# Kernel tuning notes

Hardware: AMD Instinct MI355X
Metric: run time of the kernel (lower is better)

The kernel has to match this reference:

```python
import jax, jax.numpy as jnp
import numpy as np

B, T, C = 2, 2048, 2048
H, KV, D = 16, 4, 128   # n_head, n_kv_head, head_dim
EPS = 1.1920929e-07     # torch.finfo(float32).eps, F.rms_norm default


def setup_inputs() -> dict:
    key = jax.random.key(0)
    ks = jax.random.split(key, 7)
    x = jax.random.normal(ks[0], (B, T, C), dtype=jnp.float32)
    # rope angles: cos/sin of positions, broadcastable to [B,T,H,D//2]
    inv_freq = 1.0 / (10000.0 ** (jnp.arange(0, D // 2, dtype=jnp.float32) / (D // 2)))
    ang = jnp.arange(T, dtype=jnp.float32)[:, None] * inv_freq[None, :]
    cos = jnp.cos(ang)[None, :, None, :]  # [1,T,1,D/2]
    sin = jnp.sin(ang)[None, :, None, :]
    s = 0.02
    Wq = jax.random.normal(ks[1], (C, H * D), dtype=jnp.float32) * s
    Wk = jax.random.normal(ks[2], (C, KV * D), dtype=jnp.float32) * s
    Wv = jax.random.normal(ks[3], (C, KV * D), dtype=jnp.float32) * s
    Wo = jax.random.normal(ks[4], (C, C), dtype=jnp.float32) * s
    return {"x": x, "cos": cos, "sin": sin, "Wq": Wq, "Wk": Wk, "Wv": Wv, "Wo": Wo}


def _rope(t, cos, sin):
    d = t.shape[-1] // 2
    t1, t2 = t[..., :d], t[..., d:]
    return jnp.concatenate([t1 * cos + t2 * sin, -t1 * sin + t2 * cos], axis=-1)


def _rmsnorm(t):
    return t * jax.lax.rsqrt(jnp.mean(t * t, axis=-1, keepdims=True) + EPS)


def reference(x, cos, sin, Wq, Wk, Wv, Wo):
    q = (x @ Wq).reshape(B, T, H, D)
    k = (x @ Wk).reshape(B, T, KV, D)
    v = (x @ Wv).reshape(B, T, KV, D)
    q = _rmsnorm(_rope(q, cos, sin))
    k = _rmsnorm(_rope(k, cos, sin))
    # [B, KV, G, T, D] query grouped per kv head (GQA)
    G = H // KV
    qh = q.transpose(0, 2, 1, 3).reshape(B, KV, G, T, D)
    kh = k.transpose(0, 2, 1, 3)  # [B, KV, T, D]
    vh = v.transpose(0, 2, 1, 3)
    scale = 1.0 / np.sqrt(D).astype(np.float32)
    scores = jnp.einsum('bhgqd,bhkd->bhgqk', qh, kh) * scale
    causal = jnp.tril(jnp.ones((T, T), dtype=bool))
    scores = jnp.where(causal, scores, jnp.finfo(scores.dtype).min)
    attn = jax.nn.softmax(scores, axis=-1)
    y = jnp.einsum('bhgqk,bhkd->bhgqd', attn, vh)  # [B,KV,G,T,D]
    y = y.reshape(B, H, T, D).transpose(0, 2, 1, 3).reshape(B, T, C)
    return y @ Wo
```

## Files before the change

### kernel.cpp

```cpp
#include <hip/hip_runtime.h>

using bf16x8 = __attribute__((ext_vector_type(8))) short;
using f32x4  = __attribute__((ext_vector_type(4))) float;

#define B_  2
#define T_  2048
#define C_  2048
#define H_  16
#define KV_ 4
#define D_  128

__device__ __forceinline__ unsigned short f2b(float f) {
  union { float f; unsigned int u; } v; v.f = f;
  unsigned int r = v.u + 0x7fffu + ((v.u >> 16) & 1u);
  return (unsigned short)(r >> 16);
}
__device__ __forceinline__ float b2f(unsigned short u) {
  union { unsigned int u; float f; } v; v.u = ((unsigned int)u) << 16;
  return v.f;
}
__device__ __forceinline__ unsigned int cvt_pk_bf16(float lo, float hi) {
  unsigned int r;
  asm("v_cvt_pk_bf16_f32 %0, %1, %2" : "=v"(r) : "v"(lo), "v"(hi));
  return r;
}
__device__ __forceinline__ void gld_lds16(const void* g, void* l) {
  __builtin_amdgcn_global_load_lds(
      (__attribute__((address_space(1))) void*)g,
      (__attribute__((address_space(3))) void*)l, 16, 0, 0);
}

__global__ void cast_bf16_k(const float* __restrict__ in, unsigned short* __restrict__ out) {
  int i = blockIdx.x * 256 + threadIdx.x;
  float4 f = ((const float4*)in)[i];
  ushort4 u; u.x = f2b(f.x); u.y = f2b(f.y); u.z = f2b(f.z); u.w = f2b(f.w);
  ((ushort4*)out)[i] = u;
}

__global__ void wtrans(const float* __restrict__ W, unsigned short* __restrict__ Wt,
                       int K, int N) {
  __shared__ float s[32][33];
  int n0 = blockIdx.x * 32, k0 = blockIdx.y * 32;
  int tx = threadIdx.x, ty = threadIdx.y;
  #pragma unroll
  for (int yy = 0; yy < 32; yy += 8)
    s[ty + yy][tx] = W[(size_t)(k0 + ty + yy) * N + n0 + tx];
  __syncthreads();
  #pragma unroll
  for (int yy = 0; yy < 32; yy += 8)
    Wt[(size_t)(n0 + ty + yy) * K + k0 + tx] = f2b(s[tx][ty + yy]);
}

template <bool OUT_BF16>
__device__ __forceinline__ void gemm_tile(
    const unsigned short* __restrict__ A, const unsigned short* __restrict__ Bt,
    void* __restrict__ Cv, int K, int ldc, int m0, int n0b, int n0c,
    unsigned short* sA, unsigned short* sB)
{
  const int tid  = threadIdx.x;
  const int lane = tid & 63, w = tid >> 6;
  const int quad = lane >> 4, l16 = lane & 15;
  const int wm = (w >> 1) * 64, wn = (w & 1) * 64;

  f32x4 acc[4][4] = {};

  const unsigned short* Abase = A  + (size_t)m0  * K;
  const unsigned short* Bbase = Bt + (size_t)n0b * K;

  for (int k0 = 0; k0 < K; k0 += 32) {
    #pragma unroll
    for (int r = 0; r < 2; ++r) {
      int c = tid + r * 256;
      int row = c >> 2, col = (c & 3) * 8;
      gld_lds16(Abase + (size_t)row * K + k0 + col, sA + c * 8);
      gld_lds16(Bbase + (size_t)row * K + k0 + col, sB + c * 8);
    }
    __syncthreads();
    bf16x8 af[4], bfr[4];
    #pragma unroll
    for (int i = 0; i < 4; ++i)
      af[i]  = *(const bf16x8*)(sA + (wm + i * 16 + l16) * 32 + quad * 8);
    #pragma unroll
    for (int j = 0; j < 4; ++j)
      bfr[j] = *(const bf16x8*)(sB + (wn + j * 16 + l16) * 32 + quad * 8);
    #pragma unroll
    for (int i = 0; i < 4; ++i)
      #pragma unroll
      for (int j = 0; j < 4; ++j)
        acc[i][j] = __builtin_amdgcn_mfma_f32_16x16x32_bf16(af[i], bfr[j], acc[i][j], 0, 0, 0);
    __syncthreads();
  }
  #pragma unroll
  for (int i = 0; i < 4; ++i) {
    #pragma unroll
    for (int r = 0; r < 4; ++r) {
      int row = m0 + wm + i * 16 + quad * 4 + r;
      #pragma unroll
      for (int j = 0; j < 4; ++j) {
        int col = n0c + wn + j * 16 + l16;
        float v = acc[i][j][r];
        if (OUT_BF16) ((unsigned short*)Cv)[(size_t)row * ldc + col] = f2b(v);
        else          ((float*)Cv)[(size_t)row * ldc + col] = v;
      }
    }
  }
}

__global__ void out_gemm(const unsigned short* __restrict__ yb,
                         const unsigned short* __restrict__ Wot,
                         float* __restrict__ out) {
  __shared__ unsigned short sA[128 * 32], sB[128 * 32];
  gemm_tile<false>(yb, Wot, out, C_, C_, blockIdx.y * 128, blockIdx.x * 128, blockIdx.x * 128,
                   sA, sB);
}

__global__ __launch_bounds__(512, 2) void qkv_gemm8(
    const unsigned short* __restrict__ xb,
    const unsigned short* __restrict__ Wqt,
    const unsigned short* __restrict__ Wkt,
    const unsigned short* __restrict__ Wvt,
    unsigned short* __restrict__ q, unsigned short* __restrict__ k,
    unsigned short* __restrict__ v) {
  __shared__ unsigned short lds[65536];

  const int id  = (int)blockIdx.x;
  const int xcd = id & 7, jj = id >> 3;
  const int mt  = xcd * 2 + jj / 12;
  const int nt  = jj % 12;

  const unsigned short* Bt; unsigned short* Cp; int n0, ldc;
  if (nt < 8)       { Bt = Wqt; Cp = q; n0 = nt * 256;        ldc = 2048; }
  else if (nt < 10) { Bt = Wkt; Cp = k; n0 = (nt - 8) * 256;  ldc = 512;  }
  else              { Bt = Wvt; Cp = v; n0 = (nt - 10) * 256; ldc = 512;  }
  const int m0 = mt * 256;

  const int tid = (int)threadIdx.x;
  const int w = tid >> 6, lane = tid & 63;
  const int quad = lane >> 4, l16 = lane & 15;
  const int wr = w >> 2, wc = w & 3;
  const int swz = (l16 & 12) << 1;

  const unsigned short* Ab = xb + (size_t)m0 * 2048;
  const unsigned short* Bb = Bt + (size_t)n0 * 2048;

  const int c0 = tid, c1 = tid + 512;
  const int r0 = c0 >> 2, r1 = c1 >> 2;
  const int x0 = ((c0 & 3) * 8) ^ (((c0 >> 4) & 3) << 3);
  const int x1 = ((c1 & 3) * 8) ^ (((c1 >> 4) & 3) << 3);

#define STAGE_A(buf, kh, kb) do { \
    unsigned short* d_ = lds + (buf) * 16384 + (kh) * 8192; \
    gld_lds16(Ab + (size_t)r0 * 2048 + (kb) + (kh) * 32 + x0, d_ + c0 * 8); \
    gld_lds16(Ab + (size_t)r1 * 2048 + (kb) + (kh) * 32 + x1, d_ + c1 * 8); \
  } while (0)
#define STAGE_B(buf, kh, kb) do { \
    unsigned short* d_ = lds + 32768 + (buf) * 16384 + (kh) * 8192; \
    gld_lds16(Bb + (size_t)r0 * 2048 + (kb) + (kh) * 32 + x0, d_ + c0 * 8); \
    gld_lds16(Bb + (size_t)r1 * 2048 + (kb) + (kh) * 32 + x1, d_ + c1 * 8); \
  } while (0)

  f32x4 acc[8][4] = {};

  STAGE_A(0, 0, 0); STAGE_B(0, 0, 0); STAGE_A(0, 1, 0); STAGE_B(0, 1, 0);
  asm volatile("s_waitcnt vmcnt(4)" ::: "memory");
  __builtin_amdgcn_s_barrier();

  const unsigned short* aLd = lds + (wr * 128 + l16) * 32 + (quad * 8 ^ swz);
  const unsigned short* bLd = lds + 32768 + (wc * 64 + l16) * 32 + (quad * 8 ^ swz);

  for (int t = 0; t < 32; ++t) {
    const int cur = t & 1, nxt = cur ^ 1;
    const bool more = (t < 31);
    const int kb = (t + 1) * 64;
    const int off = cur * 16384;
    bf16x8 a[8], bbr[4];

    #pragma unroll
    for (int m = 0; m < 8; ++m) a[m] = *(const bf16x8*)(aLd + off + m * 512);
    #pragma unroll
    for (int n = 0; n < 4; ++n) bbr[n] = *(const bf16x8*)(bLd + off + n * 512);
    if (more) STAGE_A(nxt, 0, kb);
    __builtin_amdgcn_s_barrier();
    asm volatile("s_waitcnt lgkmcnt(0)" ::: "memory");
    __builtin_amdgcn_sched_barrier(0);
    __builtin_amdgcn_s_setprio(1);
    #pragma unroll
    for (int m = 0; m < 4; ++m)
      #pragma unroll
      for (int n = 0; n < 4; ++n)
        acc[m][n] = __builtin_amdgcn_mfma_f32_16x16x32_bf16(a[m], bbr[n], acc[m][n], 0, 0, 0);
    __builtin_amdgcn_s_setprio(0);
    __builtin_amdgcn_s_barrier();

    if (more) STAGE_B(nxt, 0, kb);
    __builtin_amdgcn_s_barrier();
    __builtin_amdgcn_s_setprio(1);
    #pragma unroll
    for (int m = 4; m < 8; ++m)
      #pragma unroll
      for (int n = 0; n < 4; ++n)
        acc[m][n] = __builtin_amdgcn_mfma_f32_16x16x32_bf16(a[m], bbr[n], acc[m][n], 0, 0, 0);
    __builtin_amdgcn_s_setprio(0);
    if (more) asm volatile("s_waitcnt vmcnt(4)" ::: "memory");
    else      asm volatile("s_waitcnt vmcnt(0)" ::: "memory");
    __builtin_amdgcn_s_barrier();

    #pragma unroll
    for (int m = 0; m < 8; ++m) a[m] = *(const bf16x8*)(aLd + off + 8192 + m * 512);
    #pragma unroll
    for (int n = 0; n < 4; ++n) bbr[n] = *(const bf16x8*)(bLd + off + 8192 + n * 512);
    if (more) STAGE_A(nxt, 1, kb);
    __builtin_amdgcn_s_barrier();
    asm volatile("s_waitcnt lgkmcnt(0)" ::: "memory");
    __builtin_amdgcn_sched_barrier(0);
    __builtin_amdgcn_s_setprio(1);
    #pragma unroll
    for (int m = 0; m < 4; ++m)
      #pragma unroll
      for (int n = 0; n < 4; ++n)
        acc[m][n] = __builtin_amdgcn_mfma_f32_16x16x32_bf16(a[m], bbr[n], acc[m][n], 0, 0, 0);
    __builtin_amdgcn_s_setprio(0);
    __builtin_amdgcn_s_barrier();

    if (more) STAGE_B(nxt, 1, kb);
    __builtin_amdgcn_s_barrier();
    __builtin_amdgcn_s_setprio(1);
    #pragma unroll
    for (int m = 4; m < 8; ++m)
      #pragma unroll
      for (int n = 0; n < 4; ++n)
        acc[m][n] = __builtin_amdgcn_mfma_f32_16x16x32_bf16(a[m], bbr[n], acc[m][n], 0, 0, 0);
    __builtin_amdgcn_s_setprio(0);
    if (more) asm volatile("s_waitcnt vmcnt(4)" ::: "memory");
    else      asm volatile("s_waitcnt vmcnt(0)" ::: "memory");
    __builtin_amdgcn_s_barrier();
  }
#undef STAGE_A
#undef STAGE_B

  #pragma unroll
  for (int m = 0; m < 8; ++m)
    #pragma unroll
    for (int r = 0; r < 4; ++r) {
      int row = m0 + wr * 128 + m * 16 + quad * 4 + r;
      #pragma unroll
      for (int n = 0; n < 4; ++n) {
        int col = n0 + wc * 64 + n * 16 + l16;
        Cp[(size_t)row * ldc + col] = f2b(acc[m][n][r]);
      }
    }
}

template <int NH>
__global__ void ropenorm(const unsigned short* __restrict__ in,
                         const float* __restrict__ cs, const float* __restrict__ sn,
                         unsigned short* __restrict__ out, float oscale) {
  int row  = blockIdx.x * 4 + (threadIdx.x >> 6);
  int lane = threadIdx.x & 63;
  int head = row % NH;
  int t = (row / NH) & (T_ - 1);
  int b = row / (NH * T_);
  const unsigned short* p = in + (size_t)row * D_;
  float t1 = b2f(p[lane]), t2 = b2f(p[lane + 64]);
  float c = cs[t * 64 + lane], s = sn[t * 64 + lane];
  float o1 = t1 * c + t2 * s;
  float o2 = t2 * c - t1 * s;
  float ss = o1 * o1 + o2 * o2;
  #pragma unroll
  for (int off = 32; off > 0; off >>= 1) ss += __shfl_xor(ss, off, 64);
  float r = rsqrtf(ss * (1.0f / 128.0f) + 1.1920929e-07f) * oscale;
  size_t base = ((size_t)((b * NH + head) * 128 + (t >> 4))) * 2048 + (size_t)(t & 15) * 8;
  out[base + (size_t)(lane >> 3) * 128 + (lane & 7)]       = f2b(o1 * r);
  out[base + (size_t)(8 + (lane >> 3)) * 128 + (lane & 7)] = f2b(o2 * r);
}

__global__ void vfrag_k(const unsigned short* __restrict__ v, unsigned short* __restrict__ vf) {
  int it = blockIdx.x;
  int b = blockIdx.y >> 2, kv = blockIdx.y & 3;
  int d = threadIdx.x, ty = threadIdx.y;
  int t0 = it * 64;
  size_t obase = ((size_t)((b * KV_ + kv) * 32 + it)) * 8192
               + (size_t)(d >> 4) * 1024 + (size_t)(d & 15) * 8;
  #pragma unroll
  for (int tcg = 0; tcg < 4; ++tcg) {
    int tc = ty * 4 + tcg;
    unsigned short val[8];
    #pragma unroll
    for (int e = 0; e < 8; ++e)
      val[e] = v[(((size_t)(b * T_) + t0 + tc * 8 + e) * KV_ + kv) * D_ + d];
    ushort4 u0 = {val[0], val[1], val[2], val[3]};
    ushort4 u1 = {val[4], val[5], val[6], val[7]};
    *(ushort4*)(vf + obase + (size_t)tc * 128)     = u0;
    *(ushort4*)(vf + obase + (size_t)tc * 128 + 4) = u1;
  }
}

__global__ __launch_bounds__(256, 2) void attn_kernel(
    const unsigned short* __restrict__ qf, const unsigned short* __restrict__ kf,
    const unsigned short* __restrict__ vf, unsigned short* __restrict__ yb) {
  __shared__ __align__(16) char smem[34048];

  const int xp = (int)blockIdx.x;
  const int b = xp >> 2, kv = xp & 3;
  const int yp = (int)blockIdx.y;
  const int j = yp >> 2, hp = yp & 3;
  const int tid = threadIdx.x;
  const int w = tid >> 6, lane = tid & 63;
  const int quad = lane >> 4, l16 = lane & 15;
  const int qsel = w & 1, half = w >> 1;
  const int qt = qsel ? (63 - j) : j;
  const int h = kv * 4 + hp;
  const int q0 = qt * 32;
  const int ntile = (qt >> 1) + 1;
  unsigned short* myP = (unsigned short*)smem + w * (32 * 72);

  const unsigned short* Qf = qf + ((size_t)(b * H_ + h) * 128 + qt * 2) * 2048;
  const unsigned short* Kf = kf + (size_t)(b * KV_ + kv) * 128 * 2048;
  const unsigned short* Vf = vf + (size_t)(b * KV_ + kv) * 32 * 8192;

  bf16x8 bq[2][4];
  #pragma unroll
  for (int i = 0; i < 2; ++i)
    #pragma unroll
    for (int kk = 0; kk < 4; ++kk)
      bq[i][kk] = *(const bf16x8*)(Qf + (size_t)i * 2048 + (kk * 4 + quad) * 128 + l16 * 8);

  float l_i[2] = {0.f, 0.f};
  f32x4 o[2][8] = {};

  for (int it = half; it < ntile; it += 2) {
    const int t0 = it * 64;
    const unsigned short* Kt = Kf + (size_t)(it * 4) * 2048;
    const unsigned short* Vt = Vf + (size_t)it * 8192;

    f32x4 sc[4][2] = {};
    #pragma unroll
    for (int kk = 0; kk < 4; ++kk) {
      bf16x8 ak[4];
      #pragma unroll
      for (int jt = 0; jt < 4; ++jt)
        ak[jt] = *(const bf16x8*)(Kt + (size_t)jt * 2048 + (kk * 4 + quad) * 128 + l16 * 8);
      #pragma unroll
      for (int jt = 0; jt < 4; ++jt)
        #pragma unroll
        for (int i = 0; i < 2; ++i)
          sc[jt][i] = __builtin_amdgcn_mfma_f32_16x16x32_bf16(ak[jt], bq[i][kk], sc[jt][i], 0, 0, 0);
    }

    bf16x8 bv[2][8];
    #pragma unroll
    for (int kk2 = 0; kk2 < 2; ++kk2)
      #pragma unroll
      for (int jj = 0; jj < 8; ++jj)
        bv[kk2][jj] = *(const bf16x8*)(Vt + (size_t)jj * 1024 + (kk2 * 4 + quad) * 128 + l16 * 8);

    if (it == ntile - 1) {
      #pragma unroll
      for (int jt = 0; jt < 4; ++jt) {
        int kg = t0 + jt * 16 + quad * 4;
        #pragma unroll
        for (int i = 0; i < 2; ++i) {
          int qg = q0 + i * 16 + l16;
          #pragma unroll
          for (int r = 0; r < 4; ++r)
            if (kg + r > qg) sc[jt][i][r] = -3.0e38f;
        }
      }
    }

    #pragma unroll
    for (int i = 0; i < 2; ++i) {
      float part = 0.f;
      #pragma unroll
      for (int jt = 0; jt < 4; ++jt)
        #pragma unroll
        for (int r = 0; r < 4; ++r) {
          float p = __expf(sc[jt][i][r] - 12.0f);
          sc[jt][i][r] = p; part += p;
        }
      l_i[i] += part;
    }

    #pragma unroll
    for (int i = 0; i < 2; ++i)
      #pragma unroll
      for (int jt = 0; jt < 4; ++jt) {
        uint2 uu;
        uu.x = cvt_pk_bf16(sc[jt][i][0], sc[jt][i][1]);
        uu.y = cvt_pk_bf16(sc[jt][i][2], sc[jt][i][3]);
        *(uint2*)(myP + (i * 16 + l16) * 72 + jt * 16 + quad * 4) = uu;
      }

    #pragma unroll
    for (int kk2 = 0; kk2 < 2; ++kk2) {
      bf16x8 ap[2];
      #pragma unroll
      for (int i = 0; i < 2; ++i)
        ap[i] = *(const bf16x8*)(myP + (i * 16 + l16) * 72 + kk2 * 32 + quad * 8);
      #pragma unroll
      for (int i = 0; i < 2; ++i)
        #pragma unroll
        for (int jj = 0; jj < 8; ++jj)
          o[i][jj] = __builtin_amdgcn_mfma_f32_16x16x32_bf16(ap[i], bv[kk2][jj], o[i][jj], 0, 0, 0);
    }
  }

  float lsum[2];
  #pragma unroll
  for (int i = 0; i < 2; ++i) {
    float l = l_i[i];
    l += __shfl_xor(l, 16, 64);
    l += __shfl_xor(l, 32, 64);
    lsum[i] = l;
  }

  __syncthreads();
  float* oc = (float*)smem + qsel * (32 * 132);
  float* lc = (float*)smem + 2 * (32 * 132) + qsel * 32;
  if (half == 1) {
    #pragma unroll
    for (int i = 0; i < 2; ++i) {
      if (quad == 0) lc[i * 16 + l16] = lsum[i];
      #pragma unroll
      for (int jj = 0; jj < 8; ++jj)
        #pragma unroll
        for (int r = 0; r < 4; ++r)
          oc[(i * 16 + quad * 4 + r) * 132 + jj * 16 + l16] = o[i][jj][r];
    }
  }
  __syncthreads();
  if (half == 0) {
    #pragma unroll
    for (int i = 0; i < 2; ++i) {
      float l = lsum[i] + lc[i * 16 + l16];
      float linv = 1.0f / l;
      float lr[4];
      #pragma unroll
      for (int r = 0; r < 4; ++r) lr[r] = __shfl(linv, quad * 4 + r, 64);
      #pragma unroll
      for (int r = 0; r < 4; ++r) {
        int tg = q0 + i * 16 + quad * 4 + r;
        unsigned short* yr = yb + (((size_t)(b * T_ + tg)) * H_ + h) * D_;
        #pragma unroll
        for (int jj = 0; jj < 8; ++jj) {
          float vsum = o[i][jj][r] + oc[(i * 16 + quad * 4 + r) * 132 + jj * 16 + l16];
          yr[jj * 16 + l16] = f2b(vsum * lr[r]);
        }
      }
    }
  }
}

extern "C" void kernel_launch(void* const* d_in, const int* in_sizes, int n_in,
                              void* d_out, int out_size, void* d_ws, size_t ws_size,
                              hipStream_t stream) {
  (void)in_sizes; (void)n_in; (void)out_size; (void)ws_size;
  const float* x  = (const float*)d_in[0];
  const float* cs = (const float*)d_in[1];
  const float* sn = (const float*)d_in[2];
  const float* Wq = (const float*)d_in[3];
  const float* Wk = (const float*)d_in[4];
  const float* Wv = (const float*)d_in[5];
  const float* Wo = (const float*)d_in[6];
  float* out = (float*)d_out;
  char* ws = (char*)d_ws;

  unsigned short* xb   = (unsigned short*)(ws + 0);
  unsigned short* Wqt  = (unsigned short*)(ws + 16777216);
  unsigned short* Wkt  = (unsigned short*)(ws + 25165824);
  unsigned short* Wvt  = (unsigned short*)(ws + 27262976);
  unsigned short* Wot  = (unsigned short*)(ws + 29360128);
  unsigned short* qraw = (unsigned short*)(ws + 37748736);
  unsigned short* kraw = (unsigned short*)(ws + 54525952);
  unsigned short* vraw = (unsigned short*)(ws + 58720256);
  unsigned short* qfr  = (unsigned short*)(ws + 62914560);
  unsigned short* kfr  = (unsigned short*)(ws + 79691776);
  unsigned short* vfr  = (unsigned short*)(ws + 83886080);
  unsigned short* yb   = qraw;

  cast_bf16_k<<<dim3(8192), dim3(256), 0, stream>>>(x, xb);
  wtrans<<<dim3(64, 64), dim3(32, 8), 0, stream>>>(Wq, Wqt, 2048, 2048);
  wtrans<<<dim3(16, 64), dim3(32, 8), 0, stream>>>(Wk, Wkt, 2048, 512);
  wtrans<<<dim3(16, 64), dim3(32, 8), 0, stream>>>(Wv, Wvt, 2048, 512);
  wtrans<<<dim3(64, 64), dim3(32, 8), 0, stream>>>(Wo, Wot, 2048, 2048);
  qkv_gemm8<<<dim3(192), dim3(512), 0, stream>>>(xb, Wqt, Wkt, Wvt, qraw, kraw, vraw);
  ropenorm<16><<<dim3(16384), dim3(256), 0, stream>>>(qraw, cs, sn, qfr, 0.08838834764831845f);
  ropenorm<4><<<dim3(4096),  dim3(256), 0, stream>>>(kraw, cs, sn, kfr, 1.0f);
  vfrag_k<<<dim3(32, 8), dim3(128, 2), 0, stream>>>(vraw, vfr);
  attn_kernel<<<dim3(8, 128), dim3(256), 0, stream>>>(qfr, kfr, vfr, yb);
  out_gemm<<<dim3(16, 32), dim3(256), 0, stream>>>(yb, Wot, out);
}
```

Baseline: 323.5 us.

## Merge weight transposes, restructure QKV GEMM staging, vectorize rope-norm

Replaces four weight-transpose launches with a single kernel that dispatches on block index. In the QKV GEMM main loop, all four next-stage global-to-LDS loads are issued together at the start of each half-iteration, and the MFMA blocks are merged so several barriers disappear, with the vmcnt wait raised to 8. The rope+rmsnorm kernel now loads packed bf16 pairs, takes the partner half via a lane shuffle, and writes packed 32-bit results. This cuts launch overhead and barrier stalls, but issuing more loads in flight and using fewer barriers may change LDS hazard timing and register pressure.

```diff
diff --git a/kernel.cpp b/kernel.cpp
--- a/kernel.cpp
+++ b/kernel.cpp
@@ -37,10 +37,19 @@
   ((ushort4*)out)[i] = u;
 }
 
-__global__ void wtrans(const float* __restrict__ W, unsigned short* __restrict__ Wt,
-                       int K, int N) {
+__global__ void wtrans4(const float* __restrict__ Wq, const float* __restrict__ Wk,
+                        const float* __restrict__ Wv, const float* __restrict__ Wo,
+                        unsigned short* __restrict__ Wqt, unsigned short* __restrict__ Wkt,
+                        unsigned short* __restrict__ Wvt, unsigned short* __restrict__ Wot) {
   __shared__ float s[32][33];
-  int n0 = blockIdx.x * 32, k0 = blockIdx.y * 32;
+  int id = blockIdx.x;
+  const float* W; unsigned short* Wt; int N;
+  if (id < 4096)      { W = Wq; Wt = Wqt; N = 2048; }
+  else if (id < 5120) { W = Wk; Wt = Wkt; N = 512;  id -= 4096; }
+  else if (id < 6144) { W = Wv; Wt = Wvt; N = 512;  id -= 5120; }
+  else                { W = Wo; Wt = Wot; N = 2048; id -= 6144; }
+  int ntiles = N >> 5;
+  int n0 = (id % ntiles) * 32, k0 = (id / ntiles) * 32;
   int tx = threadIdx.x, ty = threadIdx.y;
   #pragma unroll
   for (int yy = 0; yy < 32; yy += 8)
@@ -48,7 +57,7 @@
   __syncthreads();
   #pragma unroll
   for (int yy = 0; yy < 32; yy += 8)
-    Wt[(size_t)(n0 + ty + yy) * K + k0 + tx] = f2b(s[tx][ty + yy]);
+    Wt[(size_t)(n0 + ty + yy) * 2048 + k0 + tx] = f2b(s[tx][ty + yy]);
 }
 
 template <bool OUT_BF16>
@@ -179,29 +188,20 @@
     for (int m = 0; m < 8; ++m) a[m] = *(const bf16x8*)(aLd + off + m * 512);
     #pragma unroll
     for (int n = 0; n < 4; ++n) bbr[n] = *(const bf16x8*)(bLd + off + n * 512);
-    if (more) STAGE_A(nxt, 0, kb);
-    __builtin_amdgcn_s_barrier();
+    if (more) {
+      STAGE_A(nxt, 0, kb); STAGE_B(nxt, 0, kb);
+      STAGE_A(nxt, 1, kb); STAGE_B(nxt, 1, kb);
+    }
     asm volatile("s_waitcnt lgkmcnt(0)" ::: "memory");
     __builtin_amdgcn_sched_barrier(0);
     __builtin_amdgcn_s_setprio(1);
     #pragma unroll
-    for (int m = 0; m < 4; ++m)
+    for (int m = 0; m < 8; ++m)
       #pragma unroll
       for (int n = 0; n < 4; ++n)
         acc[m][n] = __builtin_amdgcn_mfma_f32_16x16x32_bf16(a[m], bbr[n], acc[m][n], 0, 0, 0);
     __builtin_amdgcn_s_setprio(0);
-    __builtin_amdgcn_s_barrier();
-
-    if (more) STAGE_B(nxt, 0, kb);
-    __builtin_amdgcn_s_barrier();
-    __builtin_amdgcn_s_setprio(1);
-    #pragma unroll
-    for (int m = 4; m < 8; ++m)
-      #pragma unroll
-      for (int n = 0; n < 4; ++n)
-        acc[m][n] = __builtin_amdgcn_mfma_f32_16x16x32_bf16(a[m], bbr[n], acc[m][n], 0, 0, 0);
-    __builtin_amdgcn_s_setprio(0);
-    if (more) asm volatile("s_waitcnt vmcnt(4)" ::: "memory");
+    if (more) asm volatile("s_waitcnt vmcnt(8)" ::: "memory");
     else      asm volatile("s_waitcnt vmcnt(0)" ::: "memory");
     __builtin_amdgcn_s_barrier();
 
@@ -209,24 +209,11 @@
     for (int m = 0; m < 8; ++m) a[m] = *(const bf16x8*)(aLd + off + 8192 + m * 512);
     #pragma unroll
     for (int n = 0; n < 4; ++n) bbr[n] = *(const bf16x8*)(bLd + off + 8192 + n * 512);
-    if (more) STAGE_A(nxt, 1, kb);
-    __builtin_amdgcn_s_barrier();
     asm volatile("s_waitcnt lgkmcnt(0)" ::: "memory");
     __builtin_amdgcn_sched_barrier(0);
     __builtin_amdgcn_s_setprio(1);
     #pragma unroll
-    for (int m = 0; m < 4; ++m)
-      #pragma unroll
-      for (int n = 0; n < 4; ++n)
-        acc[m][n] = __builtin_amdgcn_mfma_f32_16x16x32_bf16(a[m], bbr[n], acc[m][n], 0, 0, 0);
-    __builtin_amdgcn_s_setprio(0);
-    __builtin_amdgcn_s_barrier();
-
-    if (more) STAGE_B(nxt, 1, kb);
-    __builtin_amdgcn_s_barrier();
-    __builtin_amdgcn_s_setprio(1);
-    #pragma unroll
-    for (int m = 4; m < 8; ++m)
+    for (int m = 0; m < 8; ++m)
       #pragma unroll
       for (int n = 0; n < 4; ++n)
         acc[m][n] = __builtin_amdgcn_mfma_f32_16x16x32_bf16(a[m], bbr[n], acc[m][n], 0, 0, 0);
@@ -261,17 +248,24 @@
   int t = (row / NH) & (T_ - 1);
   int b = row / (NH * T_);
   const unsigned short* p = in + (size_t)row * D_;
-  float t1 = b2f(p[lane]), t2 = b2f(p[lane + 64]);
-  float c = cs[t * 64 + lane], s = sn[t * 64 + lane];
-  float o1 = t1 * c + t2 * s;
-  float o2 = t2 * c - t1 * s;
-  float ss = o1 * o1 + o2 * o2;
+  unsigned int u  = *(const unsigned int*)(p + 2 * lane);
+  unsigned int up = (unsigned int)__shfl_xor((int)u, 32, 64);
+  int dh = (lane & 31) * 2;
+  float2 c2 = ((const float2*)(cs + t * 64))[lane & 31];
+  float2 s2 = ((const float2*)(sn + t * 64))[lane & 31];
+  float a0 = b2f((unsigned short)(u & 0xffff)),  a1 = b2f((unsigned short)(u >> 16));
+  float p0 = b2f((unsigned short)(up & 0xffff)), p1 = b2f((unsigned short)(up >> 16));
+  float sgn = (lane < 32) ? 1.0f : -1.0f;
+  float oa = a0 * c2.x + sgn * p0 * s2.x;
+  float ob = a1 * c2.y + sgn * p1 * s2.y;
+  float ss = oa * oa + ob * ob;
   #pragma unroll
   for (int off = 32; off > 0; off >>= 1) ss += __shfl_xor(ss, off, 64);
   float r = rsqrtf(ss * (1.0f / 128.0f) + 1.1920929e-07f) * oscale;
+  unsigned int outu = cvt_pk_bf16(oa * r, ob * r);
   size_t base = ((size_t)((b * NH + head) * 128 + (t >> 4))) * 2048 + (size_t)(t & 15) * 8;
-  out[base + (size_t)(lane >> 3) * 128 + (lane & 7)]       = f2b(o1 * r);
-  out[base + (size_t)(8 + (lane >> 3)) * 128 + (lane & 7)] = f2b(o2 * r);
+  int f = ((lane < 32) ? 0 : 8) + (dh >> 3);
+  *(unsigned int*)(out + base + (size_t)f * 128 + (dh & 7)) = outu;
 }
 
 __global__ void vfrag_k(const unsigned short* __restrict__ v, unsigned short* __restrict__ vf) {
@@ -479,10 +473,7 @@
   unsigned short* yb   = qraw;
 
   cast_bf16_k<<<dim3(8192), dim3(256), 0, stream>>>(x, xb);
-  wtrans<<<dim3(64, 64), dim3(32, 8), 0, stream>>>(Wq, Wqt, 2048, 2048);
-  wtrans<<<dim3(16, 64), dim3(32, 8), 0, stream>>>(Wk, Wkt, 2048, 512);
-  wtrans<<<dim3(16, 64), dim3(32, 8), 0, stream>>>(Wv, Wvt, 2048, 512);
-  wtrans<<<dim3(64, 64), dim3(32, 8), 0, stream>>>(Wo, Wot, 2048, 2048);
+  wtrans4<<<dim3(10240), dim3(32, 8), 0, stream>>>(Wq, Wk, Wv, Wo, Wqt, Wkt, Wvt, Wot);
   qkv_gemm8<<<dim3(192), dim3(512), 0, stream>>>(xb, Wqt, Wkt, Wvt, qraw, kraw, vraw);
   ropenorm<16><<<dim3(16384), dim3(256), 0, stream>>>(qraw, cs, sn, qfr, 0.08838834764831845f);
   ropenorm<4><<<dim3(4096),  dim3(256), 0, stream>>>(kraw, cs, sn, kfr, 1.0f);
```

Result: no change. 318.9 us (-1.4%).
